# Performance work log

Measured on AMD Instinct MI355X. Metric: run time of the kernel, lower is better.

The kernel has to match this reference:

```python
import jax, jax.numpy as jnp
import numpy as np

B, D, M, W, R, NW = 64, 512, 1024, 64, 4, 1
EPS = 1e-6


def setup_inputs() -> dict:
    key = jax.random.key(0)
    ks = jax.random.split(key, 26)
    outs = {'wv': NW * W, 'ev': NW * W, 'fg': R, 'ag': NW, 'wg': NW,
            'rm': R * (1 + 2 * NW), 'ws': NW, 'rs': R, 'wk': NW * W, 'rk': R * W}
    d = {}
    for i, (name, o) in enumerate(outs.items()):
        d[name + '_w'] = jax.random.normal(ks[2 * i], (D, o), jnp.float32) / np.sqrt(D)
        d[name + '_b'] = jax.random.normal(ks[2 * i + 1], (o,), jnp.float32) * 0.1
    d['x'] = jax.random.normal(ks[20], (B, D), jnp.float32)
    d['prev_memory'] = jax.random.normal(ks[21], (B, M, W), jnp.float32)
    d['prev_read_weights'] = jax.nn.softmax(jax.random.normal(ks[22], (B, R, M), jnp.float32), -1)
    d['prev_write_weights'] = jax.nn.softmax(jax.random.normal(ks[23], (B, NW, M), jnp.float32), -1)
    d['prev_link'] = jnp.zeros((B, NW, M, M), jnp.float32)
    d['prev_precedence'] = jnp.zeros((B, NW, M), jnp.float32)
    d['prev_usage'] = jax.random.uniform(ks[24], (B, M), jnp.float32)
    return d


def _cosine_weights(memory, keys, strengths):
    # memory [b,M,W], keys [b,H,W], strengths [b,H] (softplus already applied)
    dot = jnp.einsum('bhw,bmw->bhm', keys, memory)
    mn = jnp.sqrt(jnp.sum(memory * memory, -1) + EPS)   # [b,M]
    kn = jnp.sqrt(jnp.sum(keys * keys, -1) + EPS)       # [b,H]
    sim = dot / (kn[:, :, None] * mn[:, None, :])
    return jax.nn.softmax(sim * strengths[..., None], axis=-1)


def _allocation(usage):
    # usage [b,M] -> allocation weights [b,M] (DNC Freeness)
    usage = EPS + (1.0 - EPS) * usage
    idx = jnp.argsort(usage, axis=-1)                       # ascending usage
    sorted_usage = jnp.take_along_axis(usage, idx, -1)
    excl_cumprod = jnp.concatenate(
        [jnp.ones_like(sorted_usage[:, :1]),
         jnp.cumprod(sorted_usage, axis=-1)[:, :-1]], axis=-1)
    sorted_alloc = (1.0 - sorted_usage) * excl_cumprod
    inv = jnp.argsort(idx, axis=-1)                         # invert permutation
    return jnp.take_along_axis(sorted_alloc, inv, -1)


def _write_allocation_weights(usage, write_gates):
    # write_gates [b,NW]; sequential allocation across (few) write heads
    allocs = []
    for i in range(NW):
        a = _allocation(usage)
        allocs.append(a)
        usage = usage + (1.0 - usage) * write_gates[:, i:i + 1] * a
    return jnp.stack(allocs, axis=1)  # [b,NW,M]


def _forward(x, prev_memory, prev_read_weights, prev_write_weights, prev_link,
             prev_precedence, prev_usage, wv_w, wv_b, ev_w, ev_b, fg_w, fg_b,
             ag_w, ag_b, wg_w, wg_b, rm_w, rm_b, ws_w, ws_b, rs_w, rs_b,
             wk_w, wk_b, rk_w, rk_b):
    b = x.shape[0]
    lin = lambda w, bb: x @ w + bb
    write_vectors = lin(wv_w, wv_b).reshape(b, NW, W)
    erase_vectors = jax.nn.sigmoid(lin(ev_w, ev_b)).reshape(b, NW, W)
    free_gate = jax.nn.sigmoid(lin(fg_w, fg_b))            # [b,R]
    allocation_gate = jax.nn.sigmoid(lin(ag_w, ag_b))      # [b,NW]
    write_gate = jax.nn.sigmoid(lin(wg_w, wg_b))           # [b,NW]
    read_mode = jax.nn.softmax(lin(rm_w, rm_b).reshape(b, R, 1 + 2 * NW), -1)
    write_keys = lin(wk_w, wk_b).reshape(b, NW, W)
    write_strengths = jax.nn.softplus(lin(ws_w, ws_b))     # [b,NW]
    read_keys = lin(rk_w, rk_b).reshape(b, R, W)
    read_strengths = jax.nn.softplus(lin(rs_w, rs_b))      # [b,R]

    # --- Freeness usage update ---
    write_agg = 1.0 - jnp.prod(1.0 - prev_write_weights, axis=1)   # [b,M]
    usage_after_write = prev_usage + (1.0 - prev_usage) * write_agg
    phi = jnp.prod(1.0 - free_gate[..., None] * prev_read_weights, axis=1)
    usage = usage_after_write * phi

    # --- write weights ---
    wcw = _cosine_weights(prev_memory, write_keys, write_strengths)  # [b,NW,M]
    waw = _write_allocation_weights(usage, allocation_gate * write_gate)
    ag = allocation_gate[..., None]
    wg = write_gate[..., None]
    write_weights = wg * (ag * waw + (1.0 - ag) * wcw)               # [b,NW,M]

    # --- erase and write ---
    weighted_resets = write_weights[..., None] * erase_vectors[:, :, None, :]
    reset_gate = jnp.prod(1.0 - weighted_resets, axis=1)             # [b,M,W]
    memory = prev_memory * reset_gate + jnp.einsum(
        'bwm,bwd->bmd', write_weights, write_vectors)

    # --- temporal linkage ---
    ww_sum = jnp.sum(write_weights, -1, keepdims=True)               # [b,NW,1]
    precedence = (1.0 - ww_sum) * prev_precedence + write_weights
    w_i = write_weights[..., None]          # [b,NW,M,1]
    w_j = write_weights[:, :, None, :]      # [b,NW,1,M]
    p_j = prev_precedence[:, :, None, :]    # [b,NW,1,M]
    link = (1.0 - w_i - w_j) * prev_link + w_i * p_j
    link = link * (1.0 - jnp.eye(M, dtype=link.dtype))

    # --- read weights ---
    rcw = _cosine_weights(memory, read_keys, read_strengths)         # [b,R,M]
    fwd = jnp.einsum('brj,bwij->brwi', prev_read_weights, link)
    bwd = jnp.einsum('brj,bwji->brwi', prev_read_weights, link)
    backward_mode = read_mode[:, :, :NW]
    forward_mode = read_mode[:, :, NW:2 * NW]
    content_mode = read_mode[:, :, 2 * NW]
    read_weights = (content_mode[..., None] * rcw
                    + jnp.sum(forward_mode[..., None] * fwd, axis=2)
                    + jnp.sum(backward_mode[..., None] * bwd, axis=2))
    read_words = jnp.einsum('brm,bmd->brd', read_weights, memory)
    return read_words, memory, read_weights, write_weights, link, precedence, usage


def reference(x, prev_memory, prev_read_weights, prev_write_weights, prev_link,
              prev_precedence, prev_usage, wv_w, wv_b, ev_w, ev_b, fg_w, fg_b,
              ag_w, ag_b, wg_w, wg_b, rm_w, rm_b, ws_w, ws_b, rs_w, rs_b,
              wk_w, wk_b, rk_w, rk_b):
    return _forward(x, prev_memory, prev_read_weights, prev_write_weights,
                    prev_link, prev_precedence, prev_usage, wv_w, wv_b, ev_w,
                    ev_b, fg_w, fg_b, ag_w, ag_b, wg_w, wg_b, rm_w, rm_b,
                    ws_w, ws_b, rs_w, rs_b, wk_w, wk_b, rk_w, rk_b)
```

## Files before the change

### kernel.cpp

```cpp
#include <hip/hip_runtime.h>

#define NB 64
#define ND 512
#define NM 1024
#define NR 4
#define EPSF 1e-6f

typedef float f4_t __attribute__((ext_vector_type(4)));

static const size_t O_WV    = 0;
static const size_t O_EV    = 4096;
static const size_t O_FG    = 8192;
static const size_t O_AG    = 8448;
static const size_t O_WG    = 8512;
static const size_t O_RM    = 9344;
static const size_t O_WK    = 10112;
static const size_t O_WSTR  = 14208;
static const size_t O_RK    = 14272;
static const size_t O_RSTR  = 30656;
static const size_t O_WAW   = 96448;
static const size_t O_WWGT  = 161984;
static const size_t O_PREC  = 227520;
static const size_t O_MN    = 293056;
static const size_t O_FWD   = 358592;
static const size_t O_BWDP  = 1145024;

static const size_t OO_RWORDS = 0;
static const size_t OO_MEM    = 16384;
static const size_t OO_RW     = 4210688;
static const size_t OO_WWGT   = 4472832;
static const size_t OO_LINK   = 4538368;
static const size_t OO_PREC   = 71647232;
static const size_t OO_USAGE  = 71712768;

__device__ __forceinline__ float sigm(float x) { return 1.f / (1.f + expf(-x)); }
__device__ __forceinline__ float softplus_(float x) { return fmaxf(x, 0.f) + log1pf(expf(-fabsf(x))); }

__global__ void k_controller(
    const float* __restrict__ x,
    const float* __restrict__ wv_w, const float* __restrict__ wv_b,
    const float* __restrict__ ev_w, const float* __restrict__ ev_b,
    const float* __restrict__ fg_w, const float* __restrict__ fg_b,
    const float* __restrict__ ag_w, const float* __restrict__ ag_b,
    const float* __restrict__ wg_w, const float* __restrict__ wg_b,
    const float* __restrict__ rm_w, const float* __restrict__ rm_b,
    const float* __restrict__ ws_w, const float* __restrict__ ws_b,
    const float* __restrict__ rs_w, const float* __restrict__ rs_b,
    const float* __restrict__ wk_w, const float* __restrict__ wk_b,
    const float* __restrict__ rk_w, const float* __restrict__ rk_b,
    float* __restrict__ wsb)
{
    int b = blockIdx.x;
    int c = threadIdx.x;
    __shared__ float rmraw[12];
    if (c < 471) {
        const float* wp; const float* bp; int O; int cl; int act; size_t dsto = 0;
        if (c < 64)       { wp = wv_w; bp = wv_b; O = 64;  cl = c;       act = 0; dsto = O_WV + b * 64 + cl; }
        else if (c < 128) { wp = ev_w; bp = ev_b; O = 64;  cl = c - 64;  act = 1; dsto = O_EV + b * 64 + cl; }
        else if (c < 132) { wp = fg_w; bp = fg_b; O = 4;   cl = c - 128; act = 1; dsto = O_FG + b * 4 + cl; }
        else if (c < 133) { wp = ag_w; bp = ag_b; O = 1;   cl = 0;       act = 1; dsto = O_AG + b; }
        else if (c < 134) { wp = wg_w; bp = wg_b; O = 1;   cl = 0;       act = 1; dsto = O_WG + b; }
        else if (c < 146) { wp = rm_w; bp = rm_b; O = 12;  cl = c - 134; act = 3; }
        else if (c < 147) { wp = ws_w; bp = ws_b; O = 1;   cl = 0;       act = 2; dsto = O_WSTR + b; }
        else if (c < 151) { wp = rs_w; bp = rs_b; O = 4;   cl = c - 147; act = 2; dsto = O_RSTR + b * 4 + cl; }
        else if (c < 215) { wp = wk_w; bp = wk_b; O = 64;  cl = c - 151; act = 0; dsto = O_WK + b * 64 + cl; }
        else              { wp = rk_w; bp = rk_b; O = 256; cl = c - 215; act = 0; dsto = O_RK + b * 256 + cl; }
        float acc = bp[cl];
        const float* xb = x + b * ND;
        for (int d = 0; d < ND; ++d) acc += xb[d] * wp[d * O + cl];
        if (act == 1) acc = sigm(acc);
        else if (act == 2) acc = softplus_(acc);
        if (act == 3) rmraw[cl] = acc;
        else wsb[dsto] = acc;
    }
    __syncthreads();
    if (c < 4) {
        float a0 = rmraw[c * 3 + 0], a1 = rmraw[c * 3 + 1], a2 = rmraw[c * 3 + 2];
        float mx = fmaxf(a0, fmaxf(a1, a2));
        float e0 = expf(a0 - mx), e1 = expf(a1 - mx), e2 = expf(a2 - mx);
        float s = e0 + e1 + e2;
        float* dst = wsb + O_RM + b * 12 + c * 3;
        dst[0] = e0 / s; dst[1] = e1 / s; dst[2] = e2 / s;
    }
}

__global__ __launch_bounds__(1024) void k_alloc(
    const float* __restrict__ pu, const float* __restrict__ prw,
    const float* __restrict__ pww, float* __restrict__ wsb, float* __restrict__ out)
{
    __shared__ float sv[1024];
    __shared__ int   si[1024];
    __shared__ float sp[1024];
    int b = blockIdx.x, t = threadIdx.x;
    int idx = b * NM + t;
    float u0 = pu[idx];
    float uaw = u0 + (1.f - u0) * pww[idx];
    float phi = 1.f;
#pragma unroll
    for (int r = 0; r < NR; r++)
        phi *= (1.f - wsb[O_FG + b * 4 + r] * prw[(b * 4 + r) * NM + t]);
    float u = uaw * phi;
    out[OO_USAGE + idx] = u;
    sv[t] = EPSF + (1.0f - EPSF) * u;
    si[t] = t;
    __syncthreads();
    for (int k = 2; k <= 1024; k <<= 1) {
        for (int j = k >> 1; j > 0; j >>= 1) {
            int ixj = t ^ j;
            if (ixj > t) {
                float a = sv[t], c = sv[ixj];
                int ia = si[t], ic = si[ixj];
                bool asc = (t & k) == 0;
                bool gt = (a > c) || (a == c && ia > ic);
                if (gt == asc) { sv[t] = c; sv[ixj] = a; si[t] = ic; si[ixj] = ia; }
            }
            __syncthreads();
        }
    }
    sp[t] = sv[t];
    __syncthreads();
    for (int off = 1; off < 1024; off <<= 1) {
        float v = sp[t];
        float o = (t >= off) ? sp[t - off] : 1.f;
        __syncthreads();
        sp[t] = v * o;
        __syncthreads();
    }
    float excl = (t == 0) ? 1.f : sp[t - 1];
    wsb[O_WAW + b * NM + si[t]] = (1.f - sv[t]) * excl;
}

__global__ __launch_bounds__(256) void k_writew(
    const float* __restrict__ pm, const float* __restrict__ pp,
    float* __restrict__ wsb, float* __restrict__ out)
{
    int b = blockIdx.x, t = threadIdx.x;
    __shared__ float red[256];
    const float* wk = wsb + O_WK + b * 64;
    float kn2 = 0.f;
#pragma unroll
    for (int w = 0; w < 64; w++) { float v = wk[w]; kn2 += v * v; }
    float kn = sqrtf(kn2 + EPSF);
    float wstr = wsb[O_WSTR + b];
    float sim[4];
#pragma unroll
    for (int k = 0; k < 4; k++) {
        int m = t + k * 256;
        const float* row = pm + ((size_t)(b * NM + m)) * 64;
        float dot = 0.f, mn2 = 0.f;
        for (int w = 0; w < 64; w++) { float pv = row[w]; dot += wk[w] * pv; mn2 += pv * pv; }
        sim[k] = dot / (kn * sqrtf(mn2 + EPSF)) * wstr;
    }
    float lm = fmaxf(fmaxf(sim[0], sim[1]), fmaxf(sim[2], sim[3]));
    red[t] = lm; __syncthreads();
    for (int s = 128; s > 0; s >>= 1) { if (t < s) red[t] = fmaxf(red[t], red[t + s]); __syncthreads(); }
    float mx = red[0]; __syncthreads();
    float e[4]; float ls = 0.f;
#pragma unroll
    for (int k = 0; k < 4; k++) { e[k] = expf(sim[k] - mx); ls += e[k]; }
    red[t] = ls; __syncthreads();
    for (int s = 128; s > 0; s >>= 1) { if (t < s) red[t] += red[t + s]; __syncthreads(); }
    float inv = 1.f / red[0]; __syncthreads();
    float ag = wsb[O_AG + b], wg = wsb[O_WG + b];
    float wwv[4]; float lsum = 0.f;
#pragma unroll
    for (int k = 0; k < 4; k++) {
        int m = t + k * 256;
        float wcw = e[k] * inv;
        float waw = wsb[O_WAW + b * NM + m];
        float w_ = wg * (ag * waw + (1.f - ag) * wcw);
        wwv[k] = w_; lsum += w_;
        wsb[O_WWGT + b * NM + m] = w_;
        out[OO_WWGT + b * NM + m] = w_;
    }
    red[t] = lsum; __syncthreads();
    for (int s = 128; s > 0; s >>= 1) { if (t < s) red[t] += red[t + s]; __syncthreads(); }
    float wwsum = red[0];
#pragma unroll
    for (int k = 0; k < 4; k++) {
        int m = t + k * 256;
        float pr = (1.f - wwsum) * pp[b * NM + m] + wwv[k];
        wsb[O_PREC + b * NM + m] = pr;
        out[OO_PREC + b * NM + m] = pr;
    }
    const float* evp = wsb + O_EV + b * 64;
    const float* wvp = wsb + O_WV + b * 64;
#pragma unroll
    for (int k = 0; k < 4; k++) {
        int m = t + k * 256;
        float w_ = wwv[k];
        const float* pmr = pm + ((size_t)(b * NM + m)) * 64;
        float* outr = out + OO_MEM + ((size_t)(b * NM + m)) * 64;
        float s2 = 0.f;
        for (int w = 0; w < 64; w++) {
            float val = pmr[w] * (1.f - w_ * evp[w]) + w_ * wvp[w];
            outr[w] = val;
            s2 += val * val;
        }
        wsb[O_MN + b * NM + m] = sqrtf(s2 + EPSF);
    }
}

__global__ __launch_bounds__(256) void k_linkfb(
    const float* __restrict__ pl, const float* __restrict__ pp,
    const float* __restrict__ prw, float* __restrict__ wsb, float* __restrict__ out)
{
    int b = blockIdx.x, rg = blockIdx.y;
    int t = threadIdx.x, wave = t >> 6, lane = t & 63;
    const float* wwb = wsb + O_WWGT + b * NM;
    const float* ppb = pp + b * NM;
    const float* rwb = prw + (size_t)b * 4 * NM;
    f4_t wj[4], pj[4], rwc[4][4];
#pragma unroll
    for (int s = 0; s < 4; s++) {
        int c4 = s * 256 + lane * 4;
        wj[s] = *(const f4_t*)(wwb + c4);
        pj[s] = *(const f4_t*)(ppb + c4);
#pragma unroll
        for (int h = 0; h < 4; h++)
            rwc[h][s] = *(const f4_t*)(rwb + h * NM + c4);
    }
    f4_t bacc[4][4];
#pragma unroll
    for (int h = 0; h < 4; h++)
#pragma unroll
        for (int s = 0; s < 4; s++) bacc[h][s] = (f4_t){0.f, 0.f, 0.f, 0.f};

    int rowbase = rg * 64 + wave * 16;
    f4_t vin[4];
    {
        const float* pr0 = pl + ((size_t)(b * NM + rowbase)) * NM;
#pragma unroll
        for (int s = 0; s < 4; s++)
            vin[s] = __builtin_nontemporal_load((const f4_t*)(pr0 + s * 256 + lane * 4));
    }
    for (int rr = 0; rr < 16; rr++) {
        int row = rowbase + rr;
        f4_t vc[4];
#pragma unroll
        for (int s = 0; s < 4; s++) vc[s] = vin[s];
        if (rr < 15) {
            const float* pn = pl + ((size_t)(b * NM + row + 1)) * NM;
#pragma unroll
            for (int s = 0; s < 4; s++)
                vin[s] = __builtin_nontemporal_load((const f4_t*)(pn + s * 256 + lane * 4));
        }
        float wi = wwb[row];
        float rh0 = rwb[0 * NM + row], rh1 = rwb[1 * NM + row];
        float rh2 = rwb[2 * NM + row], rh3 = rwb[3 * NM + row];
        float a = 1.f - wi;
        float* lkrow = out + OO_LINK + ((size_t)(b * NM + row)) * NM;
        float f0 = 0.f, f1 = 0.f, f2 = 0.f, f3 = 0.f;
#pragma unroll
        for (int s = 0; s < 4; s++) {
            int c4 = s * 256 + lane * 4;
            f4_t lv;
            lv.x = (a - wj[s].x) * vc[s].x + wi * pj[s].x; if (row == c4)     lv.x = 0.f;
            lv.y = (a - wj[s].y) * vc[s].y + wi * pj[s].y; if (row == c4 + 1) lv.y = 0.f;
            lv.z = (a - wj[s].z) * vc[s].z + wi * pj[s].z; if (row == c4 + 2) lv.z = 0.f;
            lv.w = (a - wj[s].w) * vc[s].w + wi * pj[s].w; if (row == c4 + 3) lv.w = 0.f;
            __builtin_nontemporal_store(lv, (f4_t*)(lkrow + c4));
            f0 += rwc[0][s].x * lv.x + rwc[0][s].y * lv.y + rwc[0][s].z * lv.z + rwc[0][s].w * lv.w;
            f1 += rwc[1][s].x * lv.x + rwc[1][s].y * lv.y + rwc[1][s].z * lv.z + rwc[1][s].w * lv.w;
            f2 += rwc[2][s].x * lv.x + rwc[2][s].y * lv.y + rwc[2][s].z * lv.z + rwc[2][s].w * lv.w;
            f3 += rwc[3][s].x * lv.x + rwc[3][s].y * lv.y + rwc[3][s].z * lv.z + rwc[3][s].w * lv.w;
            bacc[0][s].x += rh0 * lv.x; bacc[0][s].y += rh0 * lv.y; bacc[0][s].z += rh0 * lv.z; bacc[0][s].w += rh0 * lv.w;
            bacc[1][s].x += rh1 * lv.x; bacc[1][s].y += rh1 * lv.y; bacc[1][s].z += rh1 * lv.z; bacc[1][s].w += rh1 * lv.w;
            bacc[2][s].x += rh2 * lv.x; bacc[2][s].y += rh2 * lv.y; bacc[2][s].z += rh2 * lv.z; bacc[2][s].w += rh2 * lv.w;
            bacc[3][s].x += rh3 * lv.x; bacc[3][s].y += rh3 * lv.y; bacc[3][s].z += rh3 * lv.z; bacc[3][s].w += rh3 * lv.w;
        }
#pragma unroll
        for (int off = 32; off > 0; off >>= 1) {
            f0 += __shfl_down(f0, off); f1 += __shfl_down(f1, off);
            f2 += __shfl_down(f2, off); f3 += __shfl_down(f3, off);
        }
        if (lane == 0) {
            f4_t fv = (f4_t){f0, f1, f2, f3};
            *(f4_t*)(wsb + O_FWD + (size_t)(b * NM + row) * 4) = fv;
        }
    }
    __shared__ float redb[4][1024];
#pragma unroll
    for (int h = 0; h < 4; h++) {
        __syncthreads();
#pragma unroll
        for (int s = 0; s < 4; s++)
            *(f4_t*)(&redb[wave][s * 256 + lane * 4]) = bacc[h][s];
        __syncthreads();
        for (int i = t; i < 1024; i += 256) {
            float sum = redb[0][i] + redb[1][i] + redb[2][i] + redb[3][i];
            wsb[O_BWDP + ((size_t)((b * 16 + rg) * 4 + h)) * NM + i] = sum;
        }
    }
}

__global__ __launch_bounds__(256) void k_readw(
    float* __restrict__ wsb, float* __restrict__ out)
{
    int br = blockIdx.x;
    int b = br >> 2, r = br & 3, t = threadIdx.x;
    __shared__ float red[256];
    __shared__ float vv[1024];
    __shared__ float red2[4][64];
    const float* rk = wsb + O_RK + (b * 4 + r) * 64;
    float kn2 = 0.f;
#pragma unroll
    for (int w = 0; w < 64; w++) { float v = rk[w]; kn2 += v * v; }
    float kn = sqrtf(kn2 + EPSF);
    float rstr = wsb[O_RSTR + b * 4 + r];
    float sim[4];
#pragma unroll
    for (int k = 0; k < 4; k++) {
        int m = t + k * 256;
        const float* row = out + OO_MEM + ((size_t)(b * NM + m)) * 64;
        float dot = 0.f;
        for (int w = 0; w < 64; w++) dot += rk[w] * row[w];
        sim[k] = dot / (kn * wsb[O_MN + b * NM + m]) * rstr;
    }
    float lm = fmaxf(fmaxf(sim[0], sim[1]), fmaxf(sim[2], sim[3]));
    red[t] = lm; __syncthreads();
    for (int s = 128; s > 0; s >>= 1) { if (t < s) red[t] = fmaxf(red[t], red[t + s]); __syncthreads(); }
    float mx = red[0]; __syncthreads();
    float e[4]; float ls = 0.f;
#pragma unroll
    for (int k = 0; k < 4; k++) { e[k] = expf(sim[k] - mx); ls += e[k]; }
    red[t] = ls; __syncthreads();
    for (int s = 128; s > 0; s >>= 1) { if (t < s) red[t] += red[t + s]; __syncthreads(); }
    float inv = 1.f / red[0];
    float bm = wsb[O_RM + b * 12 + r * 3 + 0];
    float fm = wsb[O_RM + b * 12 + r * 3 + 1];
    float cm = wsb[O_RM + b * 12 + r * 3 + 2];
#pragma unroll
    for (int k = 0; k < 4; k++) {
        int m = t + k * 256;
        float p = e[k] * inv;
        float bw = 0.f;
#pragma unroll
        for (int rg = 0; rg < 16; rg++)
            bw += wsb[O_BWDP + ((size_t)((b * 16 + rg) * 4 + r)) * NM + m];
        float fw = wsb[O_FWD + (size_t)(b * NM + m) * 4 + r];
        float v = cm * p + fm * fw + bm * bw;
        vv[m] = v;
        out[OO_RW + (size_t)(b * 4 + r) * NM + m] = v;
    }
    __syncthreads();
    int w = t & 63, chunk = t >> 6;
    const float* mem = out + OO_MEM + (size_t)b * NM * 64;
    float acc = 0.f;
    int m0 = chunk * 256;
    for (int m = m0; m < m0 + 256; m++)
        acc += vv[m] * mem[(size_t)m * 64 + w];
    red2[chunk][w] = acc;
    __syncthreads();
    if (t < 64)
        out[OO_RWORDS + br * 64 + t] = red2[0][t] + red2[1][t] + red2[2][t] + red2[3][t];
}

extern "C" void kernel_launch(void* const* d_in, const int* in_sizes, int n_in,
                              void* d_out, int out_size, void* d_ws, size_t ws_size,
                              hipStream_t stream) {
    const float* wv_w = (const float*)d_in[0];  const float* wv_b = (const float*)d_in[1];
    const float* ev_w = (const float*)d_in[2];  const float* ev_b = (const float*)d_in[3];
    const float* fg_w = (const float*)d_in[4];  const float* fg_b = (const float*)d_in[5];
    const float* ag_w = (const float*)d_in[6];  const float* ag_b = (const float*)d_in[7];
    const float* wg_w = (const float*)d_in[8];  const float* wg_b = (const float*)d_in[9];
    const float* rm_w = (const float*)d_in[10]; const float* rm_b = (const float*)d_in[11];
    const float* ws_w = (const float*)d_in[12]; const float* ws_b = (const float*)d_in[13];
    const float* rs_w = (const float*)d_in[14]; const float* rs_b = (const float*)d_in[15];
    const float* wk_w = (const float*)d_in[16]; const float* wk_b = (const float*)d_in[17];
    const float* rk_w = (const float*)d_in[18]; const float* rk_b = (const float*)d_in[19];
    const float* x   = (const float*)d_in[20];
    const float* pm  = (const float*)d_in[21];
    const float* prw = (const float*)d_in[22];
    const float* pww = (const float*)d_in[23];
    const float* pl  = (const float*)d_in[24];
    const float* pp  = (const float*)d_in[25];
    const float* pu  = (const float*)d_in[26];
    float* out = (float*)d_out;
    float* wsb = (float*)d_ws;

    k_controller<<<NB, 512, 0, stream>>>(x, wv_w, wv_b, ev_w, ev_b, fg_w, fg_b, ag_w, ag_b,
                                         wg_w, wg_b, rm_w, rm_b, ws_w, ws_b, rs_w, rs_b,
                                         wk_w, wk_b, rk_w, rk_b, wsb);
    k_alloc<<<NB, 1024, 0, stream>>>(pu, prw, pww, wsb, out);
    k_writew<<<NB, 256, 0, stream>>>(pm, pp, wsb, out);
    k_linkfb<<<dim3(NB, 16), 256, 0, stream>>>(pl, pp, prw, wsb, out);
    k_readw<<<NB * NR, 256, 0, stream>>>(wsb, out);
}
```

Baseline: 224.8 us.

## Fuse controller, allocation sort and write-weight kernels into one block-per-batch kernel

Merges the controller projection, usage/allocation bitonic sort and write-weighting/memory-update kernels into a single 1024-thread kernel per batch. Intermediate values (controller outputs, allocation weights) now stay in shared memory instead of going through the global workspace. The write-weighting stage now runs one memory row per thread across 1024 threads instead of four rows per thread across 256. This removes two launches and the workspace round trips between them. In exchange, the fused block uses more shared memory, and its longer barrier chains run on only 64 blocks.

```diff
diff --git a/kernel.cpp b/kernel.cpp
--- a/kernel.cpp
+++ b/kernel.cpp
@@ -8,19 +8,10 @@
 
 typedef float f4_t __attribute__((ext_vector_type(4)));
 
-static const size_t O_WV    = 0;
-static const size_t O_EV    = 4096;
-static const size_t O_FG    = 8192;
-static const size_t O_AG    = 8448;
-static const size_t O_WG    = 8512;
 static const size_t O_RM    = 9344;
-static const size_t O_WK    = 10112;
-static const size_t O_WSTR  = 14208;
 static const size_t O_RK    = 14272;
 static const size_t O_RSTR  = 30656;
-static const size_t O_WAW   = 96448;
 static const size_t O_WWGT  = 161984;
-static const size_t O_PREC  = 227520;
 static const size_t O_MN    = 293056;
 static const size_t O_FWD   = 358592;
 static const size_t O_BWDP  = 1145024;
@@ -36,7 +27,7 @@
 __device__ __forceinline__ float sigm(float x) { return 1.f / (1.f + expf(-x)); }
 __device__ __forceinline__ float softplus_(float x) { return fmaxf(x, 0.f) + log1pf(expf(-fabsf(x))); }
 
-__global__ void k_controller(
+__global__ __launch_bounds__(1024) void k_front(
     const float* __restrict__ x,
     const float* __restrict__ wv_w, const float* __restrict__ wv_b,
     const float* __restrict__ ev_w, const float* __restrict__ ev_b,
@@ -48,62 +39,77 @@
     const float* __restrict__ rs_w, const float* __restrict__ rs_b,
     const float* __restrict__ wk_w, const float* __restrict__ wk_b,
     const float* __restrict__ rk_w, const float* __restrict__ rk_b,
-    float* __restrict__ wsb)
+    const float* __restrict__ pm,  const float* __restrict__ pp,
+    const float* __restrict__ pu,  const float* __restrict__ prw,
+    const float* __restrict__ pww,
+    float* __restrict__ wsb, float* __restrict__ out)
 {
-    int b = blockIdx.x;
-    int c = threadIdx.x;
-    __shared__ float rmraw[12];
-    if (c < 471) {
-        const float* wp; const float* bp; int O; int cl; int act; size_t dsto = 0;
-        if (c < 64)       { wp = wv_w; bp = wv_b; O = 64;  cl = c;       act = 0; dsto = O_WV + b * 64 + cl; }
-        else if (c < 128) { wp = ev_w; bp = ev_b; O = 64;  cl = c - 64;  act = 1; dsto = O_EV + b * 64 + cl; }
-        else if (c < 132) { wp = fg_w; bp = fg_b; O = 4;   cl = c - 128; act = 1; dsto = O_FG + b * 4 + cl; }
-        else if (c < 133) { wp = ag_w; bp = ag_b; O = 1;   cl = 0;       act = 1; dsto = O_AG + b; }
-        else if (c < 134) { wp = wg_w; bp = wg_b; O = 1;   cl = 0;       act = 1; dsto = O_WG + b; }
-        else if (c < 146) { wp = rm_w; bp = rm_b; O = 12;  cl = c - 134; act = 3; }
-        else if (c < 147) { wp = ws_w; bp = ws_b; O = 1;   cl = 0;       act = 2; dsto = O_WSTR + b; }
-        else if (c < 151) { wp = rs_w; bp = rs_b; O = 4;   cl = c - 147; act = 2; dsto = O_RSTR + b * 4 + cl; }
-        else if (c < 215) { wp = wk_w; bp = wk_b; O = 64;  cl = c - 151; act = 0; dsto = O_WK + b * 64 + cl; }
-        else              { wp = rk_w; bp = rk_b; O = 256; cl = c - 215; act = 0; dsto = O_RK + b * 256 + cl; }
+    int b = blockIdx.x, t = threadIdx.x;
+    __shared__ float sv[1024];
+    __shared__ int   si[1024];
+    __shared__ float sp[1024];
+    __shared__ float red[1024];
+    __shared__ float swaw[1024];
+    __shared__ float cl_wv[64], cl_ev[64], cl_wk[64], cl_fg[4], rmraw[12];
+    __shared__ float cl_scal[3];
+
+    if (t < 471) {
+        int c = t;
+        const float* wp; const float* bp; int O; int cl;
+        int act; int dst;
+        if (c < 64)       { wp = wv_w; bp = wv_b; O = 64;  cl = c;       act = 0; dst = 0; }
+        else if (c < 128) { wp = ev_w; bp = ev_b; O = 64;  cl = c - 64;  act = 1; dst = 1; }
+        else if (c < 132) { wp = fg_w; bp = fg_b; O = 4;   cl = c - 128; act = 1; dst = 2; }
+        else if (c < 133) { wp = ag_w; bp = ag_b; O = 1;   cl = 0;       act = 1; dst = 3; }
+        else if (c < 134) { wp = wg_w; bp = wg_b; O = 1;   cl = 0;       act = 1; dst = 4; }
+        else if (c < 146) { wp = rm_w; bp = rm_b; O = 12;  cl = c - 134; act = 0; dst = 5; }
+        else if (c < 147) { wp = ws_w; bp = ws_b; O = 1;   cl = 0;       act = 2; dst = 6; }
+        else if (c < 151) { wp = rs_w; bp = rs_b; O = 4;   cl = c - 147; act = 2; dst = 7; }
+        else if (c < 215) { wp = wk_w; bp = wk_b; O = 64;  cl = c - 151; act = 0; dst = 8; }
+        else              { wp = rk_w; bp = rk_b; O = 256; cl = c - 215; act = 0; dst = 9; }
         float acc = bp[cl];
         const float* xb = x + b * ND;
         for (int d = 0; d < ND; ++d) acc += xb[d] * wp[d * O + cl];
         if (act == 1) acc = sigm(acc);
         else if (act == 2) acc = softplus_(acc);
-        if (act == 3) rmraw[cl] = acc;
-        else wsb[dsto] = acc;
-    }
-    __syncthreads();
-    if (c < 4) {
-        float a0 = rmraw[c * 3 + 0], a1 = rmraw[c * 3 + 1], a2 = rmraw[c * 3 + 2];
+        switch (dst) {
+            case 0: cl_wv[cl] = acc; break;
+            case 1: cl_ev[cl] = acc; break;
+            case 2: cl_fg[cl] = acc; break;
+            case 3: cl_scal[0] = acc; break;
+            case 4: cl_scal[1] = acc; break;
+            case 5: rmraw[cl] = acc; break;
+            case 6: cl_scal[2] = acc; break;
+            case 7: wsb[O_RSTR + b * 4 + cl] = acc; break;
+            case 8: cl_wk[cl] = acc; break;
+            default: wsb[O_RK + b * 256 + cl] = acc; break;
+        }
+    }
+    __syncthreads();
+    if (t < 4) {
+        float a0 = rmraw[t * 3 + 0], a1 = rmraw[t * 3 + 1], a2 = rmraw[t * 3 + 2];
         float mx = fmaxf(a0, fmaxf(a1, a2));
         float e0 = expf(a0 - mx), e1 = expf(a1 - mx), e2 = expf(a2 - mx);
         float s = e0 + e1 + e2;
-        float* dst = wsb + O_RM + b * 12 + c * 3;
+        float* dst = wsb + O_RM + b * 12 + t * 3;
         dst[0] = e0 / s; dst[1] = e1 / s; dst[2] = e2 / s;
     }
-}
-
-__global__ __launch_bounds__(1024) void k_alloc(
-    const float* __restrict__ pu, const float* __restrict__ prw,
-    const float* __restrict__ pww, float* __restrict__ wsb, float* __restrict__ out)
-{
-    __shared__ float sv[1024];
-    __shared__ int   si[1024];
-    __shared__ float sp[1024];
-    int b = blockIdx.x, t = threadIdx.x;
-    int idx = b * NM + t;
-    float u0 = pu[idx];
-    float uaw = u0 + (1.f - u0) * pww[idx];
-    float phi = 1.f;
-#pragma unroll
-    for (int r = 0; r < NR; r++)
-        phi *= (1.f - wsb[O_FG + b * 4 + r] * prw[(b * 4 + r) * NM + t]);
-    float u = uaw * phi;
-    out[OO_USAGE + idx] = u;
-    sv[t] = EPSF + (1.0f - EPSF) * u;
-    si[t] = t;
-    __syncthreads();
+
+    int m = t;
+    {
+        float u0 = pu[b * NM + m];
+        float uaw = u0 + (1.f - u0) * pww[b * NM + m];
+        float phi = 1.f;
+#pragma unroll
+        for (int r = 0; r < NR; r++)
+            phi *= (1.f - cl_fg[r] * prw[(b * 4 + r) * NM + m]);
+        float u = uaw * phi;
+        out[OO_USAGE + b * NM + m] = u;
+        sv[t] = EPSF + (1.0f - EPSF) * u;
+        si[t] = t;
+    }
+    __syncthreads();
+
     for (int k = 2; k <= 1024; k <<= 1) {
         for (int j = k >> 1; j > 0; j >>= 1) {
             int ixj = t ^ j;
@@ -126,79 +132,44 @@
         sp[t] = v * o;
         __syncthreads();
     }
-    float excl = (t == 0) ? 1.f : sp[t - 1];
-    wsb[O_WAW + b * NM + si[t]] = (1.f - sv[t]) * excl;
-}
-
-__global__ __launch_bounds__(256) void k_writew(
-    const float* __restrict__ pm, const float* __restrict__ pp,
-    float* __restrict__ wsb, float* __restrict__ out)
-{
-    int b = blockIdx.x, t = threadIdx.x;
-    __shared__ float red[256];
-    const float* wk = wsb + O_WK + b * 64;
+    {
+        float excl = (t == 0) ? 1.f : sp[t - 1];
+        swaw[si[t]] = (1.f - sv[t]) * excl;
+    }
+    __syncthreads();
+
     float kn2 = 0.f;
 #pragma unroll
-    for (int w = 0; w < 64; w++) { float v = wk[w]; kn2 += v * v; }
+    for (int w = 0; w < 64; w++) { float v = cl_wk[w]; kn2 += v * v; }
     float kn = sqrtf(kn2 + EPSF);
-    float wstr = wsb[O_WSTR + b];
-    float sim[4];
-#pragma unroll
-    for (int k = 0; k < 4; k++) {
-        int m = t + k * 256;
-        const float* row = pm + ((size_t)(b * NM + m)) * 64;
-        float dot = 0.f, mn2 = 0.f;
-        for (int w = 0; w < 64; w++) { float pv = row[w]; dot += wk[w] * pv; mn2 += pv * pv; }
-        sim[k] = dot / (kn * sqrtf(mn2 + EPSF)) * wstr;
-    }
-    float lm = fmaxf(fmaxf(sim[0], sim[1]), fmaxf(sim[2], sim[3]));
-    red[t] = lm; __syncthreads();
-    for (int s = 128; s > 0; s >>= 1) { if (t < s) red[t] = fmaxf(red[t], red[t + s]); __syncthreads(); }
+    const float* prow = pm + ((size_t)(b * NM + m)) * 64;
+    float dot = 0.f, mn2 = 0.f;
+    for (int w = 0; w < 64; w++) { float pv = prow[w]; dot += cl_wk[w] * pv; mn2 += pv * pv; }
+    float sim = dot / (kn * sqrtf(mn2 + EPSF)) * cl_scal[2];
+    red[t] = sim; __syncthreads();
+    for (int s = 512; s > 0; s >>= 1) { if (t < s) red[t] = fmaxf(red[t], red[t + s]); __syncthreads(); }
     float mx = red[0]; __syncthreads();
-    float e[4]; float ls = 0.f;
-#pragma unroll
-    for (int k = 0; k < 4; k++) { e[k] = expf(sim[k] - mx); ls += e[k]; }
-    red[t] = ls; __syncthreads();
-    for (int s = 128; s > 0; s >>= 1) { if (t < s) red[t] += red[t + s]; __syncthreads(); }
-    float inv = 1.f / red[0]; __syncthreads();
-    float ag = wsb[O_AG + b], wg = wsb[O_WG + b];
-    float wwv[4]; float lsum = 0.f;
-#pragma unroll
-    for (int k = 0; k < 4; k++) {
-        int m = t + k * 256;
-        float wcw = e[k] * inv;
-        float waw = wsb[O_WAW + b * NM + m];
-        float w_ = wg * (ag * waw + (1.f - ag) * wcw);
-        wwv[k] = w_; lsum += w_;
-        wsb[O_WWGT + b * NM + m] = w_;
-        out[OO_WWGT + b * NM + m] = w_;
-    }
-    red[t] = lsum; __syncthreads();
-    for (int s = 128; s > 0; s >>= 1) { if (t < s) red[t] += red[t + s]; __syncthreads(); }
+    float e = expf(sim - mx);
+    red[t] = e; __syncthreads();
+    for (int s = 512; s > 0; s >>= 1) { if (t < s) red[t] += red[t + s]; __syncthreads(); }
+    float se = red[0]; __syncthreads();
+    float ag = cl_scal[0], wg = cl_scal[1];
+    float ww = wg * (ag * swaw[m] + (1.f - ag) * (e / se));
+    wsb[O_WWGT + b * NM + m] = ww;
+    out[OO_WWGT + b * NM + m] = ww;
+    red[t] = ww; __syncthreads();
+    for (int s = 512; s > 0; s >>= 1) { if (t < s) red[t] += red[t + s]; __syncthreads(); }
     float wwsum = red[0];
-#pragma unroll
-    for (int k = 0; k < 4; k++) {
-        int m = t + k * 256;
-        float pr = (1.f - wwsum) * pp[b * NM + m] + wwv[k];
-        wsb[O_PREC + b * NM + m] = pr;
-        out[OO_PREC + b * NM + m] = pr;
-    }
-    const float* evp = wsb + O_EV + b * 64;
-    const float* wvp = wsb + O_WV + b * 64;
-#pragma unroll
-    for (int k = 0; k < 4; k++) {
-        int m = t + k * 256;
-        float w_ = wwv[k];
-        const float* pmr = pm + ((size_t)(b * NM + m)) * 64;
-        float* outr = out + OO_MEM + ((size_t)(b * NM + m)) * 64;
-        float s2 = 0.f;
-        for (int w = 0; w < 64; w++) {
-            float val = pmr[w] * (1.f - w_ * evp[w]) + w_ * wvp[w];
-            outr[w] = val;
-            s2 += val * val;
-        }
-        wsb[O_MN + b * NM + m] = sqrtf(s2 + EPSF);
-    }
+    out[OO_PREC + b * NM + m] = (1.f - wwsum) * pp[b * NM + m] + ww;
+
+    float s2 = 0.f;
+    float* outr = out + OO_MEM + ((size_t)(b * NM + m)) * 64;
+    for (int w = 0; w < 64; w++) {
+        float val = prow[w] * (1.f - ww * cl_ev[w]) + ww * cl_wv[w];
+        outr[w] = val;
+        s2 += val * val;
+    }
+    wsb[O_MN + b * NM + m] = sqrtf(s2 + EPSF);
 }
 
 __global__ __launch_bounds__(256) void k_linkfb(
@@ -379,11 +350,10 @@
     float* out = (float*)d_out;
     float* wsb = (float*)d_ws;
 
-    k_controller<<<NB, 512, 0, stream>>>(x, wv_w, wv_b, ev_w, ev_b, fg_w, fg_b, ag_w, ag_b,
-                                         wg_w, wg_b, rm_w, rm_b, ws_w, ws_b, rs_w, rs_b,
-                                         wk_w, wk_b, rk_w, rk_b, wsb);
-    k_alloc<<<NB, 1024, 0, stream>>>(pu, prw, pww, wsb, out);
-    k_writew<<<NB, 256, 0, stream>>>(pm, pp, wsb, out);
+    k_front<<<NB, 1024, 0, stream>>>(x, wv_w, wv_b, ev_w, ev_b, fg_w, fg_b, ag_w, ag_b,
+                                     wg_w, wg_b, rm_w, rm_b, ws_w, ws_b, rs_w, rs_b,
+                                     wk_w, wk_b, rk_w, rk_b,
+                                     pm, pp, pu, prw, pww, wsb, out);
     k_linkfb<<<dim3(NB, 16), 256, 0, stream>>>(pl, pp, prw, wsb, out);
     k_readw<<<NB * NR, 256, 0, stream>>>(wsb, out);
 }
```

After: 216.7 us, median of 2. 1.04x faster.
